# Kernel optimization log

Measured on AMD Instinct MI355X. Metric: run time of the kernel, lower is better.

## Reference

```python
import jax, jax.numpy as jnp
import numpy as np

TAU = 0.1
SELF_MASK = 1e6  # added to diagonal of self-distances (y_neg is x)


def _cdist(a, b):
    # pairwise L2 distances, [Na, Nb]; eps keeps sqrt grad finite at 0
    sq = (a * a).sum(-1)[:, None] + (b * b).sum(-1)[None, :] - 2.0 * (a @ b.T)
    return jnp.sqrt(jnp.maximum(sq, 1e-12))


def setup_inputs() -> dict:
    key = jax.random.key(0)
    k1, k2 = jax.random.split(key)
    N, D = 4096, 512
    return {
        "x": jax.random.normal(k1, (N, D), dtype=jnp.float32),
        "y_pos": jax.random.normal(k2, (N, D), dtype=jnp.float32),
    }


def reference(x, y_pos):
    # compute_drift_velocity with y_neg = x (training/loss path)
    N = x.shape[0]
    dist_pos = _cdist(x, y_pos)                      # [N, N]
    dist_neg = _cdist(x, x) + SELF_MASK * jnp.eye(N, dtype=x.dtype)
    logits = -jnp.concatenate([dist_pos, dist_neg], axis=1) / TAU  # [N, 2N]
    # dual normalization: row softmax * column softmax, geometric mean
    A_row = jax.nn.softmax(logits, axis=-1)
    A_col = jax.nn.softmax(logits, axis=0)
    A = jnp.sqrt(A_row * A_col)
    A_pos, A_neg = A[:, :N], A[:, N:]
    drift = A_pos @ y_pos - A_neg @ x                # [N, D]
    return drift
```

## Files before the change

### kernel.cpp

```cpp
#include <hip/hip_runtime.h>
#include <math.h>

#define NN   4096
#define DD   512
#define TWON 8192
#define KSLICE 4

typedef _Float16 half_t;
using half8 = __attribute__((ext_vector_type(8))) half_t;
using f32x4 = __attribute__((ext_vector_type(4))) float;

__device__ __forceinline__ void gl16(const void* g, void* l) {
    __builtin_amdgcn_global_load_lds(
        (const __attribute__((address_space(1))) void*)g,
        (__attribute__((address_space(3))) void*)l, 16, 0, 0);
}
__device__ __forceinline__ f32x4 mfma16h(half8 a, half8 b, f32x4 c) {
    return __builtin_amdgcn_mfma_f32_16x16x32_f16(a, b, c, 0, 0, 0);
}

__global__ __launch_bounds__(64)
void prep_k(const float* __restrict__ x, const float* __restrict__ y,
            half_t* __restrict__ bhi, float* __restrict__ nb) {
    int r = blockIdx.x;
    int l = threadIdx.x;
    const float* src = (r < NN) ? (y + (size_t)r * DD) : (x + (size_t)(r - NN) * DD);
    float4 v0 = *reinterpret_cast<const float4*>(src + l * 8);
    float4 v1 = *reinterpret_cast<const float4*>(src + l * 8 + 4);
    float e[8] = {v0.x, v0.y, v0.z, v0.w, v1.x, v1.y, v1.z, v1.w};
    float s = 0.f;
    half8 h;
    #pragma unroll
    for (int q = 0; q < 8; ++q) {
        s += e[q] * e[q];
        h[q] = (half_t)e[q];
    }
    *reinterpret_cast<half8*>(bhi + (size_t)r * DD + l * 8) = h;
    #pragma unroll
    for (int off = 32; off; off >>= 1) s += __shfl_down(s, off);
    if (l == 0) nb[r] = s;
}

__global__ __launch_bounds__(256)
void b2t_k(const float* __restrict__ x, const float* __restrict__ y, half_t* __restrict__ b2t) {
    __shared__ float tl[32][33];
    int k0 = blockIdx.x * 32, d0 = blockIdx.y * 32;
    int tx = threadIdx.x, ty = threadIdx.y;
    const float* src = (k0 < NN) ? y : x;
    int row0 = (k0 < NN) ? k0 : (k0 - NN);
    #pragma unroll
    for (int j = 0; j < 4; ++j)
        tl[ty + 8 * j][tx] = src[(size_t)(row0 + ty + 8 * j) * DD + d0 + tx];
    __syncthreads();
    float sgn = (k0 < NN) ? 1.f : -1.f;
    #pragma unroll
    for (int j = 0; j < 4; ++j) {
        float v = tl[tx][ty + 8 * j] * sgn;
        b2t[(size_t)(d0 + ty + 8 * j) * TWON + k0 + tx] = (half_t)v;
    }
}

__global__ __launch_bounds__(256)
void gemm1_k(const half_t* __restrict__ bhi,
             const float* __restrict__ nb, half_t* __restrict__ Ef,
             float* __restrict__ rpm, float* __restrict__ rps,
             float* __restrict__ cpm, float* __restrict__ cps) {
    __shared__ unsigned char lds[32768];
    const int t = threadIdx.x;
    const int wave = t >> 6, lane = t & 63;
    const int i0 = blockIdx.y * 128, j0 = blockIdx.x * 128;
    const int wm = (wave >> 1) * 64, wn = (wave & 1) * 64;
    const half_t* ahig = bhi + (size_t)NN * DD;
    f32x4 acc[4][4] = {};
    for (int k0 = 0; k0 < DD; k0 += 64) {
        __syncthreads();
        #pragma unroll
        for (int q = 0; q < 4; ++q) {
            const int dbase = (wave * 4 + q) * 1024;
            const int p  = dbase + lane * 16;
            const int r  = p >> 7;
            const int cb = (p & 127) ^ ((r & 7) << 4);
            const size_t offA = (size_t)(i0 + r) * DD + k0 + (cb >> 1);
            const size_t offB = (size_t)(j0 + r) * DD + k0 + (cb >> 1);
            gl16(ahig + offA, lds + dbase);
            gl16(bhi  + offB, lds + 16384 + dbase);
        }
        asm volatile("s_waitcnt vmcnt(0)" ::: "memory");
        __builtin_amdgcn_sched_barrier(0);
        __syncthreads();
        #pragma unroll
        for (int kk = 0; kk < 2; ++kk) {
            half8 ah[4];
            #pragma unroll
            for (int m = 0; m < 4; ++m) {
                const int row = wm + m * 16 + (lane & 15);
                const int off = row * 128 + ((kk * 64 + (lane >> 4) * 16) ^ ((row & 7) << 4));
                ah[m] = *reinterpret_cast<const half8*>(lds + off);
            }
            #pragma unroll
            for (int n = 0; n < 4; ++n) {
                const int row = wn + n * 16 + (lane & 15);
                const int off = row * 128 + ((kk * 64 + (lane >> 4) * 16) ^ ((row & 7) << 4));
                half8 bh = *reinterpret_cast<const half8*>(lds + 16384 + off);
                #pragma unroll
                for (int m = 0; m < 4; ++m)
                    acc[m][n] = mfma16h(ah[m], bh, acc[m][n]);
            }
        }
    }
    float nbj[4];
    #pragma unroll
    for (int n = 0; n < 4; ++n) nbj[n] = nb[j0 + wn + n * 16 + (lane & 15)];
    #pragma unroll
    for (int m = 0; m < 4; ++m) {
        #pragma unroll
        for (int r4 = 0; r4 < 4; ++r4) {
            const int i = i0 + wm + m * 16 + (lane >> 4) * 4 + r4;
            const float nxi = nb[NN + i];
            #pragma unroll
            for (int n = 0; n < 4; ++n) {
                const int j = j0 + wn + n * 16 + (lane & 15);
                float sq = nxi + nbj[n] - 2.0f * acc[m][n][r4];
                float lg = -10.0f * sqrtf(fmaxf(sq, 1e-12f));
                if (j == i + NN) lg = -1e7f;
                acc[m][n][r4] = lg;
            }
        }
    }
    float rmx[16];
    #pragma unroll
    for (int m = 0; m < 4; ++m)
        #pragma unroll
        for (int r4 = 0; r4 < 4; ++r4)
            rmx[m * 4 + r4] = fmaxf(fmaxf(acc[m][0][r4], acc[m][1][r4]),
                                    fmaxf(acc[m][2][r4], acc[m][3][r4]));
    #pragma unroll
    for (int off = 1; off < 16; off <<= 1)
        #pragma unroll
        for (int idx = 0; idx < 16; ++idx)
            rmx[idx] = fmaxf(rmx[idx], __shfl_xor(rmx[idx], off));
    __syncthreads();
    float* red = reinterpret_cast<float*>(lds);
    if ((lane & 15) == 0) {
        #pragma unroll
        for (int m = 0; m < 4; ++m)
            #pragma unroll
            for (int r4 = 0; r4 < 4; ++r4) {
                const int r = wm + m * 16 + (lane >> 4) * 4 + r4;
                red[(wave & 1) * 128 + r] = rmx[m * 4 + r4];
            }
    }
    __syncthreads();
    float rmt[16];
    #pragma unroll
    for (int m = 0; m < 4; ++m)
        #pragma unroll
        for (int r4 = 0; r4 < 4; ++r4) {
            const int r = wm + m * 16 + (lane >> 4) * 4 + r4;
            rmt[m * 4 + r4] = fmaxf(rmx[m * 4 + r4], red[(((wave & 1) ^ 1)) * 128 + r]);
        }
    float rs[16] = {};
    #pragma unroll
    for (int m = 0; m < 4; ++m) {
        #pragma unroll
        for (int r4 = 0; r4 < 4; ++r4) {
            const int idx = m * 4 + r4;
            const int i = i0 + wm + m * 16 + (lane >> 4) * 4 + r4;
            #pragma unroll
            for (int n = 0; n < 4; ++n) {
                const int j = j0 + wn + n * 16 + (lane & 15);
                float e = __expf(acc[m][n][r4] - rmt[idx]);
                acc[m][n][r4] = e;
                Ef[(size_t)i * TWON + j] = (half_t)(e * 1024.0f);
                rs[idx] += e;
            }
        }
    }
    #pragma unroll
    for (int off = 1; off < 16; off <<= 1)
        #pragma unroll
        for (int idx = 0; idx < 16; ++idx) rs[idx] += __shfl_xor(rs[idx], off);
    float tmax = rmt[0];
    #pragma unroll
    for (int idx = 1; idx < 16; ++idx) tmax = fmaxf(tmax, rmt[idx]);
    tmax = fmaxf(tmax, __shfl_xor(tmax, 16));
    tmax = fmaxf(tmax, __shfl_xor(tmax, 32));
    __syncthreads();
    if (((wave & 1) == 0) && (lane & 15) == 0) {
        #pragma unroll
        for (int m = 0; m < 4; ++m)
            #pragma unroll
            for (int r4 = 0; r4 < 4; ++r4) {
                const int r = wm + m * 16 + (lane >> 4) * 4 + r4;
                red[r] = rmt[m * 4 + r4];
            }
    }
    if ((lane & 15) == 0) {
        #pragma unroll
        for (int m = 0; m < 4; ++m)
            #pragma unroll
            for (int r4 = 0; r4 < 4; ++r4) {
                const int r = wm + m * 16 + (lane >> 4) * 4 + r4;
                red[128 + (wave & 1) * 128 + r] = rs[m * 4 + r4];
            }
    }
    if (lane == 0) red[384 + wave] = tmax;
    __syncthreads();
    const float C = fmaxf(fmaxf(red[384], red[385]), fmaxf(red[386], red[387]));
    float w[16];
    #pragma unroll
    for (int idx = 0; idx < 16; ++idx) w[idx] = __expf(rmt[idx] - C);
    float cs[4] = {};
    #pragma unroll
    for (int m = 0; m < 4; ++m)
        #pragma unroll
        for (int r4 = 0; r4 < 4; ++r4)
            #pragma unroll
            for (int n = 0; n < 4; ++n)
                cs[n] = fmaf(acc[m][n][r4], w[m * 4 + r4], cs[n]);
    #pragma unroll
    for (int off = 16; off < 64; off <<= 1)
        #pragma unroll
        for (int n = 0; n < 4; ++n) cs[n] += __shfl_xor(cs[n], off);
    if (lane < 16) {
        #pragma unroll
        for (int n = 0; n < 4; ++n) {
            const int c = wn + n * 16 + lane;
            red[512 + (wave >> 1) * 128 + c] = cs[n];
        }
    }
    __syncthreads();
    if (t < 128) {
        rpm[(size_t)blockIdx.x * NN + i0 + t] = red[t];
        rps[(size_t)blockIdx.x * NN + i0 + t] = red[128 + t] + red[256 + t];
    } else {
        const int c = t - 128;
        cpm[(size_t)blockIdx.y * TWON + j0 + c] = C;
        cps[(size_t)blockIdx.y * TWON + j0 + c] = red[512 + c] + red[640 + c];
    }
}

__global__ __launch_bounds__(256)
void row_comb_k(const float* __restrict__ rpm, const float* __restrict__ rps,
                float* __restrict__ rm, float* __restrict__ rrs) {
    int i = blockIdx.x * 256 + threadIdx.x;
    float M = -3.0e38f;
    for (int tt = 0; tt < TWON / 128; ++tt) M = fmaxf(M, rpm[(size_t)tt * NN + i]);
    float S = 0.f;
    for (int tt = 0; tt < TWON / 128; ++tt)
        S += rps[(size_t)tt * NN + i] * __expf(rpm[(size_t)tt * NN + i] - M);
    rm[i] = M; rrs[i] = rsqrtf(S);
}

__global__ __launch_bounds__(256)
void col_comb_k(const float* __restrict__ cpm, const float* __restrict__ cps,
                float* __restrict__ cm, float* __restrict__ rcs) {
    int j = blockIdx.x * 256 + threadIdx.x;
    float M = -3.0e38f;
    for (int tt = 0; tt < NN / 128; ++tt) M = fmaxf(M, cpm[(size_t)tt * TWON + j]);
    float S = 0.f;
    for (int tt = 0; tt < NN / 128; ++tt)
        S += cps[(size_t)tt * TWON + j] * __expf(cpm[(size_t)tt * TWON + j] - M);
    cm[j] = M; rcs[j] = rsqrtf(S);
}

__global__ __launch_bounds__(256)
void transform_k(half_t* __restrict__ Ef, const float* __restrict__ rpm,
                 const float* __restrict__ rm,
                 const float* __restrict__ cm, const float* __restrict__ rcs) {
    const size_t nidx8 = (size_t)NN * TWON / 8;
    const size_t stride = (size_t)gridDim.x * 256;
    for (size_t idx = (size_t)blockIdx.x * 256 + threadIdx.x; idx < nidx8; idx += stride) {
        const size_t base = idx * 8;
        const int i = (int)(base >> 13);
        const int j = (int)(base & 8191);
        const int jb = j >> 7;
        const float arg0 = rpm[(size_t)jb * NN + i] - 0.5f * rm[i];
        half8 e = *reinterpret_cast<half8*>(Ef + base);
        float4 c0 = *reinterpret_cast<const float4*>(cm + j);
        float4 c1 = *reinterpret_cast<const float4*>(cm + j + 4);
        float4 r0 = *reinterpret_cast<const float4*>(rcs + j);
        float4 r1 = *reinterpret_cast<const float4*>(rcs + j + 4);
        half8 o;
        o[0] = (half_t)((float)e[0] * (__expf(arg0 - 0.5f * c0.x) * r0.x * 9.765625e-4f));
        o[1] = (half_t)((float)e[1] * (__expf(arg0 - 0.5f * c0.y) * r0.y * 9.765625e-4f));
        o[2] = (half_t)((float)e[2] * (__expf(arg0 - 0.5f * c0.z) * r0.z * 9.765625e-4f));
        o[3] = (half_t)((float)e[3] * (__expf(arg0 - 0.5f * c0.w) * r0.w * 9.765625e-4f));
        o[4] = (half_t)((float)e[4] * (__expf(arg0 - 0.5f * c1.x) * r1.x * 9.765625e-4f));
        o[5] = (half_t)((float)e[5] * (__expf(arg0 - 0.5f * c1.y) * r1.y * 9.765625e-4f));
        o[6] = (half_t)((float)e[6] * (__expf(arg0 - 0.5f * c1.z) * r1.z * 9.765625e-4f));
        o[7] = (half_t)((float)e[7] * (__expf(arg0 - 0.5f * c1.w) * r1.w * 9.765625e-4f));
        *reinterpret_cast<half8*>(Ef + base) = o;
    }
}

__global__ __launch_bounds__(512)
void gemm2_k(const half_t* __restrict__ Ef, const half_t* __restrict__ b2t,
             const float* __restrict__ rrs, float* __restrict__ part) {
    __shared__ unsigned char lds[16384];
    const int t = threadIdx.x;
    const int wave = t >> 6, lane = t & 63;
    const int sw = blockIdx.x;
    const int xcd = sw & 7;
    const int kslice = xcd >> 1;
    const int iblk = (sw >> 3) + (xcd & 1) * 32;
    const int i0 = iblk * 64;
    const int kbase = kslice * (TWON / KSLICE);
    const int wn = wave * 64;
    const int sr = t >> 3;
    const int scb = ((t & 7) * 16) ^ ((sr & 7) << 4);
    const size_t sga = (size_t)(i0 + sr) * TWON + (scb >> 1);
    const int NT = (TWON / KSLICE) / 64;
    f32x4 acc[4][4] = {};
    int cur = 0;
    gl16(Ef + sga + kbase, lds + t * 16);
    __syncthreads();
    for (int it = 0; it < NT; ++it) {
        half8 bfr0[4], bfr1[4];
        #pragma unroll
        for (int n = 0; n < 4; ++n) {
            const int d = wn + n * 16 + (lane & 15);
            const half_t* bp = b2t + (size_t)d * TWON + kbase + it * 64 + (lane >> 4) * 8;
            bfr0[n] = *reinterpret_cast<const half8*>(bp);
            bfr1[n] = *reinterpret_cast<const half8*>(bp + 32);
        }
        if (it + 1 < NT)
            gl16(Ef + sga + kbase + (it + 1) * 64, lds + ((cur ^ 1) * 8192) + t * 16);
        #pragma unroll
        for (int kk = 0; kk < 2; ++kk) {
            half8 af[4];
            #pragma unroll
            for (int m = 0; m < 4; ++m) {
                const int row = m * 16 + (lane & 15);
                const int off = cur * 8192 + row * 128 +
                                ((kk * 64 + (lane >> 4) * 16) ^ ((row & 7) << 4));
                af[m] = *reinterpret_cast<const half8*>(lds + off);
            }
            #pragma unroll
            for (int m = 0; m < 4; ++m)
                #pragma unroll
                for (int n = 0; n < 4; ++n)
                    acc[m][n] = mfma16h(af[m], (kk == 0) ? bfr0[n] : bfr1[n], acc[m][n]);
        }
        __syncthreads();
        cur ^= 1;
    }
    float* pout = part + (size_t)kslice * NN * DD;
    #pragma unroll
    for (int m = 0; m < 4; ++m) {
        float rf[4];
        #pragma unroll
        for (int r4 = 0; r4 < 4; ++r4) rf[r4] = rrs[i0 + m * 16 + (lane >> 4) * 4 + r4];
        #pragma unroll
        for (int n = 0; n < 4; ++n) {
            const int d = wn + n * 16 + (lane & 15);
            #pragma unroll
            for (int r4 = 0; r4 < 4; ++r4) {
                const int i = i0 + m * 16 + (lane >> 4) * 4 + r4;
                pout[(size_t)i * DD + d] = acc[m][n][r4] * rf[r4];
            }
        }
    }
}

__global__ __launch_bounds__(256)
void reduce_k(const float* __restrict__ part, float* __restrict__ out) {
    const size_t e4 = ((size_t)blockIdx.x * 256 + threadIdx.x) * 4;
    float4 a = *reinterpret_cast<const float4*>(part + e4);
    #pragma unroll
    for (int s = 1; s < KSLICE; ++s) {
        float4 b = *reinterpret_cast<const float4*>(part + (size_t)s * NN * DD + e4);
        a.x += b.x; a.y += b.y; a.z += b.z; a.w += b.w;
    }
    *reinterpret_cast<float4*>(out + e4) = a;
}

extern "C" void kernel_launch(void* const* d_in, const int* in_sizes, int n_in,
                              void* d_out, int out_size, void* d_ws, size_t ws_size,
                              hipStream_t stream) {
    const float* x = (const float*)d_in[0];
    const float* y = (const float*)d_in[1];
    float* out = (float*)d_out;

    char* w = (char*)d_ws;
    const size_t OFF_EF   = 0;
    const size_t OFF_BHI  = 67108864;
    const size_t OFF_B2T  = OFF_BHI + 8388608;
    const size_t OFF_PART = OFF_B2T + 8388608;
    const size_t OFF_RPM  = OFF_PART + 33554432;
    const size_t OFF_RPS  = OFF_RPM + 1048576;
    const size_t OFF_CPM  = OFF_RPS + 1048576;
    const size_t OFF_CPS  = OFF_CPM + 1048576;
    const size_t OFF_TAIL = OFF_CPS + 1048576;

    half_t* Ef   = (half_t*)(w + OFF_EF);
    half_t* bhi  = (half_t*)(w + OFF_BHI);
    half_t* b2t  = (half_t*)(w + OFF_B2T);
    float*  part = (float*)(w + OFF_PART);
    float*  rpm  = (float*)(w + OFF_RPM);
    float*  rps  = (float*)(w + OFF_RPS);
    float*  cpm  = (float*)(w + OFF_CPM);
    float*  cps  = (float*)(w + OFF_CPS);
    float*  nb   = (float*)(w + OFF_TAIL);
    float*  rm   = nb  + TWON;
    float*  rrs  = rm  + NN;
    float*  cm   = rrs + NN;
    float*  rcs  = cm  + TWON;

    prep_k<<<TWON, 64, 0, stream>>>(x, y, bhi, nb);
    gemm1_k<<<dim3(TWON / 128, NN / 128), 256, 0, stream>>>(bhi, nb, Ef,
                                                            rpm, rps, cpm, cps);
    row_comb_k<<<NN / 256, 256, 0, stream>>>(rpm, rps, rm, rrs);
    col_comb_k<<<TWON / 256, 256, 0, stream>>>(cpm, cps, cm, rcs);
    transform_k<<<2048, 256, 0, stream>>>(Ef, rpm, rm, cm, rcs);
    b2t_k<<<dim3(TWON / 32, DD / 32), dim3(32, 8), 0, stream>>>(x, y, b2t);
    gemm2_k<<<256, 512, 0, stream>>>(Ef, b2t, rrs, part);
    reduce_k<<<(NN * DD / 4) / 256, 256, 0, stream>>>(part, out);
}
```

Baseline: 213.0 us.

## Fuse softmax transform into gemm2 A-tile load and double k-slices

Removes the standalone transform pass over the 64MB half matrix by applying the dual-softmax scaling while staging A tiles into LDS inside gemm2. The column normalization is folded into a single log-domain term Pj, so each element needs one exp. K-slicing goes from 4 to 8, doubling gemm2's grid to 512 blocks and its partial-sum buffer. This trades one full read and write pass for register-path loads and exps inside the GEMM, plus a larger reduction.

```diff
diff --git a/kernel.cpp b/kernel.cpp
--- a/kernel.cpp
+++ b/kernel.cpp
@@ -4,7 +4,7 @@
 #define NN   4096
 #define DD   512
 #define TWON 8192
-#define KSLICE 4
+#define KSLICE 8
 
 typedef _Float16 half_t;
 using half8 = __attribute__((ext_vector_type(8))) half_t;
@@ -254,67 +254,61 @@
 
 __global__ __launch_bounds__(256)
 void col_comb_k(const float* __restrict__ cpm, const float* __restrict__ cps,
-                float* __restrict__ cm, float* __restrict__ rcs) {
+                float* __restrict__ Pj) {
     int j = blockIdx.x * 256 + threadIdx.x;
     float M = -3.0e38f;
     for (int tt = 0; tt < NN / 128; ++tt) M = fmaxf(M, cpm[(size_t)tt * TWON + j]);
     float S = 0.f;
     for (int tt = 0; tt < NN / 128; ++tt)
         S += cps[(size_t)tt * TWON + j] * __expf(cpm[(size_t)tt * TWON + j] - M);
-    cm[j] = M; rcs[j] = rsqrtf(S);
-}
-
-__global__ __launch_bounds__(256)
-void transform_k(half_t* __restrict__ Ef, const float* __restrict__ rpm,
-                 const float* __restrict__ rm,
-                 const float* __restrict__ cm, const float* __restrict__ rcs) {
-    const size_t nidx8 = (size_t)NN * TWON / 8;
-    const size_t stride = (size_t)gridDim.x * 256;
-    for (size_t idx = (size_t)blockIdx.x * 256 + threadIdx.x; idx < nidx8; idx += stride) {
-        const size_t base = idx * 8;
-        const int i = (int)(base >> 13);
-        const int j = (int)(base & 8191);
-        const int jb = j >> 7;
-        const float arg0 = rpm[(size_t)jb * NN + i] - 0.5f * rm[i];
-        half8 e = *reinterpret_cast<half8*>(Ef + base);
-        float4 c0 = *reinterpret_cast<const float4*>(cm + j);
-        float4 c1 = *reinterpret_cast<const float4*>(cm + j + 4);
-        float4 r0 = *reinterpret_cast<const float4*>(rcs + j);
-        float4 r1 = *reinterpret_cast<const float4*>(rcs + j + 4);
-        half8 o;
-        o[0] = (half_t)((float)e[0] * (__expf(arg0 - 0.5f * c0.x) * r0.x * 9.765625e-4f));
-        o[1] = (half_t)((float)e[1] * (__expf(arg0 - 0.5f * c0.y) * r0.y * 9.765625e-4f));
-        o[2] = (half_t)((float)e[2] * (__expf(arg0 - 0.5f * c0.z) * r0.z * 9.765625e-4f));
-        o[3] = (half_t)((float)e[3] * (__expf(arg0 - 0.5f * c0.w) * r0.w * 9.765625e-4f));
-        o[4] = (half_t)((float)e[4] * (__expf(arg0 - 0.5f * c1.x) * r1.x * 9.765625e-4f));
-        o[5] = (half_t)((float)e[5] * (__expf(arg0 - 0.5f * c1.y) * r1.y * 9.765625e-4f));
-        o[6] = (half_t)((float)e[6] * (__expf(arg0 - 0.5f * c1.z) * r1.z * 9.765625e-4f));
-        o[7] = (half_t)((float)e[7] * (__expf(arg0 - 0.5f * c1.w) * r1.w * 9.765625e-4f));
-        *reinterpret_cast<half8*>(Ef + base) = o;
-    }
-}
-
-__global__ __launch_bounds__(512)
+    Pj[j] = -0.5f * M - 0.5f * logf(S);
+}
+
+__global__ __launch_bounds__(512, 4)
 void gemm2_k(const half_t* __restrict__ Ef, const half_t* __restrict__ b2t,
-             const float* __restrict__ rrs, float* __restrict__ part) {
+             const float* __restrict__ rpm, const float* __restrict__ rm,
+             const float* __restrict__ Pj, const float* __restrict__ rrs,
+             float* __restrict__ part) {
     __shared__ unsigned char lds[16384];
     const int t = threadIdx.x;
     const int wave = t >> 6, lane = t & 63;
     const int sw = blockIdx.x;
-    const int xcd = sw & 7;
-    const int kslice = xcd >> 1;
-    const int iblk = (sw >> 3) + (xcd & 1) * 32;
-    const int i0 = iblk * 64;
+    const int kslice = sw & 7;
+    const int i0 = (sw >> 3) * 64;
     const int kbase = kslice * (TWON / KSLICE);
     const int wn = wave * 64;
     const int sr = t >> 3;
-    const int scb = ((t & 7) * 16) ^ ((sr & 7) << 4);
-    const size_t sga = (size_t)(i0 + sr) * TWON + (scb >> 1);
+    const int kc = (t & 7) * 8;
+    const int awbyte = sr * 128 + ((kc * 2) ^ ((sr & 7) << 4));
     const int NT = (TWON / KSLICE) / 64;
+    const float rmh = 0.5f * rm[i0 + sr] + 6.9314718f;
     f32x4 acc[4][4] = {};
+    half8 aE;
+    float4 p0, p1;
+    float arg;
+    auto LOADA = [&](int it) {
+        const int k = kbase + it * 64 + kc;
+        aE = *reinterpret_cast<const half8*>(Ef + (size_t)(i0 + sr) * TWON + k);
+        p0 = *reinterpret_cast<const float4*>(Pj + k);
+        p1 = *reinterpret_cast<const float4*>(Pj + k + 4);
+        arg = rpm[(size_t)((kbase + it * 64) >> 7) * NN + i0 + sr] - rmh;
+    };
+    auto STOREA = [&](int buf) {
+        half8 g;
+        g[0] = (half_t)((float)aE[0] * __expf(arg + p0.x));
+        g[1] = (half_t)((float)aE[1] * __expf(arg + p0.y));
+        g[2] = (half_t)((float)aE[2] * __expf(arg + p0.z));
+        g[3] = (half_t)((float)aE[3] * __expf(arg + p0.w));
+        g[4] = (half_t)((float)aE[4] * __expf(arg + p1.x));
+        g[5] = (half_t)((float)aE[5] * __expf(arg + p1.y));
+        g[6] = (half_t)((float)aE[6] * __expf(arg + p1.z));
+        g[7] = (half_t)((float)aE[7] * __expf(arg + p1.w));
+        *reinterpret_cast<half8*>(lds + buf * 8192 + awbyte) = g;
+    };
+    LOADA(0);
+    STOREA(0);
+    __syncthreads();
     int cur = 0;
-    gl16(Ef + sga + kbase, lds + t * 16);
-    __syncthreads();
     for (int it = 0; it < NT; ++it) {
         half8 bfr0[4], bfr1[4];
         #pragma unroll
@@ -324,8 +318,7 @@
             bfr0[n] = *reinterpret_cast<const half8*>(bp);
             bfr1[n] = *reinterpret_cast<const half8*>(bp + 32);
         }
-        if (it + 1 < NT)
-            gl16(Ef + sga + kbase + (it + 1) * 64, lds + ((cur ^ 1) * 8192) + t * 16);
+        if (it + 1 < NT) LOADA(it + 1);
         #pragma unroll
         for (int kk = 0; kk < 2; ++kk) {
             half8 af[4];
@@ -342,6 +335,7 @@
                 for (int n = 0; n < 4; ++n)
                     acc[m][n] = mfma16h(af[m], (kk == 0) ? bfr0[n] : bfr1[n], acc[m][n]);
         }
+        if (it + 1 < NT) STOREA(cur ^ 1);
         __syncthreads();
         cur ^= 1;
     }
@@ -387,7 +381,7 @@
     const size_t OFF_BHI  = 67108864;
     const size_t OFF_B2T  = OFF_BHI + 8388608;
     const size_t OFF_PART = OFF_B2T + 8388608;
-    const size_t OFF_RPM  = OFF_PART + 33554432;
+    const size_t OFF_RPM  = OFF_PART + 67108864;
     const size_t OFF_RPS  = OFF_RPM + 1048576;
     const size_t OFF_CPM  = OFF_RPS + 1048576;
     const size_t OFF_CPS  = OFF_CPM + 1048576;
@@ -404,16 +398,14 @@
     float*  nb   = (float*)(w + OFF_TAIL);
     float*  rm   = nb  + TWON;
     float*  rrs  = rm  + NN;
-    float*  cm   = rrs + NN;
-    float*  rcs  = cm  + TWON;
+    float*  Pj   = rrs + NN;
 
     prep_k<<<TWON, 64, 0, stream>>>(x, y, bhi, nb);
     gemm1_k<<<dim3(TWON / 128, NN / 128), 256, 0, stream>>>(bhi, nb, Ef,
                                                             rpm, rps, cpm, cps);
     row_comb_k<<<NN / 256, 256, 0, stream>>>(rpm, rps, rm, rrs);
-    col_comb_k<<<TWON / 256, 256, 0, stream>>>(cpm, cps, cm, rcs);
-    transform_k<<<2048, 256, 0, stream>>>(Ef, rpm, rm, cm, rcs);
+    col_comb_k<<<TWON / 256, 256, 0, stream>>>(cpm, cps, Pj);
     b2t_k<<<dim3(TWON / 32, DD / 32), dim3(32, 8), 0, stream>>>(x, y, b2t);
-    gemm2_k<<<256, 512, 0, stream>>>(Ef, b2t, rrs, part);
+    gemm2_k<<<512, 512, 0, stream>>>(Ef, b2t, rpm, rm, Pj, rrs, part);
     reduce_k<<<(NN * DD / 4) / 256, 256, 0, stream>>>(part, out);
 }
```

Measured after the change: 195.9 us. 8.0% less time.
